# Performance work log

Measured on AMD Instinct MI355X. Metric: run time of the kernel, lower is better.

The kernel has to match this reference:

```python
import jax, jax.numpy as jnp
import numpy as np
import math


def setup_inputs() -> dict:
    key = jax.random.key(0)
    k1, k2, k3 = jax.random.split(key, 3)
    B, H, T, D = 4, 16, 4096, 128
    return {
        "q": jax.random.normal(k1, (B, H, T, D), dtype=jnp.float32),
        "k": jax.random.normal(k2, (B, H, T, D), dtype=jnp.float32),
        "v": jax.random.normal(k3, (B, H, T, D), dtype=jnp.float32),
        "BS": 32,
    }


def _compress(x, block_size):
    # blockwise mean-pool along T: [B,H,T,D] -> [B,H,C,D], C = ceil(T/BS)
    B, H, T, D = x.shape
    C = math.ceil(T / block_size)
    pad = C * block_size - T
    if pad:
        x = jnp.pad(x, ((0, 0), (0, 0), (0, pad), (0, 0)))
    return x.reshape(B, H, C, block_size, D).mean(axis=3)


def reference(q, k, v, BS):
    dk = k.shape[-1]
    k_cmp = _compress(k, BS)  # [B,H,C,D]
    v_cmp = _compress(v, BS)  # [B,H,C,D]
    # scaled dot-product attention over compressed KV
    score = jnp.einsum("bhtd,bhcd->bhtc", q, k_cmp) / math.sqrt(dk)
    score = jax.nn.softmax(score, axis=-1)  # [B,H,T,C]
    out = jnp.einsum("bhtc,bhcd->bhtd", score, v_cmp)  # [B,H,T,D]
    return (out, score)
```

## Files before the change

kernel.cpp:

```cpp
#include <hip/hip_runtime.h>
#include <hip/hip_bf16.h>

typedef __attribute__((ext_vector_type(8))) short short8;
typedef __attribute__((ext_vector_type(4))) float f32x4;

#define B_  4
#define H_  16
#define T_  4096
#define D_  128
#define BS_ 32
#define C_  128
#define BH_ (B_ * H_)

__device__ __forceinline__ int posperm(int x) {
  return (x & ~31) | (((x >> 2) & 3) << 3) | (((x >> 4) & 1) << 2) | (x & 3);
}

__device__ __forceinline__ unsigned short f2bf(float f) {
  __hip_bfloat16 h = __float2bfloat16(f);
  return __builtin_bit_cast(unsigned short, h);
}

__device__ __forceinline__ void gload_lds16(const uint4* g, uint4* l) {
  __builtin_amdgcn_global_load_lds(
      (const __attribute__((address_space(1))) unsigned int*)g,
      (__attribute__((address_space(3))) unsigned int*)l, 16, 0, 0);
}

__global__ __launch_bounds__(256) void compress_kernel(
    const float* __restrict__ k, const float* __restrict__ v,
    unsigned short* __restrict__ kc, unsigned short* __restrict__ vT) {
  int blk = blockIdx.x;
  int bh  = blk >> 4;
  int cg  = blk & 15;
  int cb  = cg * 8 + (threadIdx.x >> 5);
  int l   = threadIdx.x & 31;
  const float* kp = k + ((size_t)bh * T_ + (size_t)cb * BS_) * D_ + 4 * l;
  const float* vp = v + ((size_t)bh * T_ + (size_t)cb * BS_) * D_ + 4 * l;
  float4 ks = {0.f, 0.f, 0.f, 0.f}, vs = {0.f, 0.f, 0.f, 0.f};
#pragma unroll
  for (int j = 0; j < BS_; ++j) {
    float4 a = *(const float4*)(kp + (size_t)j * D_);
    float4 b = *(const float4*)(vp + (size_t)j * D_);
    ks.x += a.x; ks.y += a.y; ks.z += a.z; ks.w += a.w;
    vs.x += b.x; vs.y += b.y; vs.z += b.z; vs.w += b.w;
  }
  const float s  = 1.0f / BS_;
  const float sk = s * 0.08838834764831845f;
  size_t slab = (size_t)bh * (C_ * D_);
  unsigned short kq[4] = {f2bf(ks.x * sk), f2bf(ks.y * sk), f2bf(ks.z * sk), f2bf(ks.w * sk)};
  int p0 = posperm(4 * l) ^ ((cb & 7) << 3);
  *(uint2*)&kc[slab + (size_t)cb * D_ + p0] = *(const uint2*)kq;
  float vv[4] = {vs.x * s, vs.y * s, vs.z * s, vs.w * s};
#pragma unroll
  for (int i = 0; i < 4; ++i) {
    int d = 4 * l + i;
    vT[slab + (size_t)d * C_ + (posperm(cb) ^ ((d & 7) << 3))] = f2bf(vv[i]);
  }
}

__global__ __launch_bounds__(256, 4) void attn_kernel(
    const float* __restrict__ q, const unsigned short* __restrict__ kc,
    const unsigned short* __restrict__ vT, float* __restrict__ out,
    float* __restrict__ score) {
  __shared__ uint4 sbuf[2048];

  int blk    = blockIdx.x;
  int bh     = blk >> 6;
  int tchunk = blk & 63;
  int tid    = threadIdx.x;
  int wave   = tid >> 6;
  int lane   = tid & 63;
  int g      = lane >> 4;
  int lr     = lane & 15;
  int rx     = lr & 7;
  int t0     = tchunk * 64 + wave * 16;

  const uint4* kg = (const uint4*)(kc + (size_t)bh * (C_ * D_));
  const uint4* vg = (const uint4*)(vT + (size_t)bh * (C_ * D_));

  const float* qrow = q + ((size_t)bh * T_ + t0 + lr) * D_;
  float4 qa[4], qb[4];
#pragma unroll
  for (int ks = 0; ks < 4; ++ks) {
    int d0 = 4 * g + 32 * ks;
    qa[ks] = *(const float4*)(qrow + d0);
    qb[ks] = *(const float4*)(qrow + d0 + 16);
  }

#pragma unroll
  for (int it = 0; it < 8; ++it) gload_lds16(&kg[it * 256 + tid], &sbuf[it * 256 + tid]);

  short8 qf[4];
#pragma unroll
  for (int ks = 0; ks < 4; ++ks) {
    short8 f;
    f[0] = (short)f2bf(qa[ks].x); f[1] = (short)f2bf(qa[ks].y);
    f[2] = (short)f2bf(qa[ks].z); f[3] = (short)f2bf(qa[ks].w);
    f[4] = (short)f2bf(qb[ks].x); f[5] = (short)f2bf(qb[ks].y);
    f[6] = (short)f2bf(qb[ks].z); f[7] = (short)f2bf(qb[ks].w);
    qf[ks] = f;
  }
  __syncthreads();

  f32x4 accS[8];
#pragma unroll
  for (int cm = 0; cm < 8; ++cm) accS[cm] = f32x4{0.f, 0.f, 0.f, 0.f};
#pragma unroll
  for (int cm = 0; cm < 8; ++cm) {
    int rbase = (lr + 16 * cm) * 16;
#pragma unroll
    for (int ks = 0; ks < 4; ++ks) {
      uint4 kf = sbuf[rbase + ((4 * ks + g) ^ rx)];
      accS[cm] = __builtin_amdgcn_mfma_f32_16x16x32_bf16(
          __builtin_bit_cast(short8, kf), qf[ks], accS[cm], 0, 0, 0);
    }
  }

  float m = -3.0e38f;
#pragma unroll
  for (int cm = 0; cm < 8; ++cm)
#pragma unroll
    for (int r = 0; r < 4; ++r) m = fmaxf(m, accS[cm][r]);
  m = fmaxf(m, __shfl_xor(m, 16));
  m = fmaxf(m, __shfl_xor(m, 32));

  float sum = 0.f;
#pragma unroll
  for (int cm = 0; cm < 8; ++cm) {
#pragma unroll
    for (int r = 0; r < 4; ++r) {
      float p = __expf(accS[cm][r] - m);
      accS[cm][r] = p;
      sum += p;
    }
  }
  sum += __shfl_xor(sum, 16);
  sum += __shfl_xor(sum, 32);
  float inv = 1.0f / sum;
#pragma unroll
  for (int cm = 0; cm < 8; ++cm)
#pragma unroll
    for (int r = 0; r < 4; ++r) accS[cm][r] *= inv;

  __syncthreads();

  float* bw = (float*)sbuf + wave * 2048;
#pragma unroll
  for (int cm = 0; cm < 8; ++cm) {
    int c4 = (g + 4 * cm) ^ rx;
    *(f32x4*)&bw[lr * 128 + c4 * 4] = accS[cm];
  }
  float* dstS = score + ((size_t)bh * T_ + t0) * C_;
#pragma unroll
  for (int j = 0; j < 8; ++j) {
    int row = 2 * j + (lane >> 5);
    int c4  = lane & 31;
    f32x4 val = *(const f32x4*)&bw[row * 128 + (c4 ^ (row & 7)) * 4];
    __builtin_nontemporal_store(val, (f32x4*)&dstS[(size_t)row * C_ + c4 * 4]);
  }

  short8 pf[4];
#pragma unroll
  for (int ks = 0; ks < 4; ++ks) {
    short8 f;
#pragma unroll
    for (int r = 0; r < 4; ++r) {
      f[r]     = (short)f2bf(accS[2 * ks][r]);
      f[4 + r] = (short)f2bf(accS[2 * ks + 1][r]);
    }
    pf[ks] = f;
  }
  __syncthreads();

#pragma unroll
  for (int it = 0; it < 8; ++it) gload_lds16(&vg[it * 256 + tid], &sbuf[it * 256 + tid]);
  __syncthreads();

  f32x4 o[8];
#pragma unroll
  for (int nt = 0; nt < 8; ++nt) o[nt] = f32x4{0.f, 0.f, 0.f, 0.f};
#pragma unroll
  for (int nt = 0; nt < 8; ++nt) {
    int rbase = (lr + 16 * nt) * 16;
#pragma unroll
    for (int ks = 0; ks < 4; ++ks) {
      uint4 vf = sbuf[rbase + ((4 * ks + g) ^ rx)];
      o[nt] = __builtin_amdgcn_mfma_f32_16x16x32_bf16(
          __builtin_bit_cast(short8, vf), pf[ks], o[nt], 0, 0, 0);
    }
  }
  __syncthreads();

#pragma unroll
  for (int nt = 0; nt < 8; ++nt) {
    int c4 = (g + 4 * nt) ^ rx;
    *(f32x4*)&bw[lr * 128 + c4 * 4] = o[nt];
  }
  float* dstO = out + ((size_t)bh * T_ + t0) * D_;
#pragma unroll
  for (int j = 0; j < 8; ++j) {
    int row = 2 * j + (lane >> 5);
    int c4  = lane & 31;
    f32x4 val = *(const f32x4*)&bw[row * 128 + (c4 ^ (row & 7)) * 4];
    __builtin_nontemporal_store(val, (f32x4*)&dstO[(size_t)row * D_ + c4 * 4]);
  }
}

extern "C" void kernel_launch(void* const* d_in, const int* in_sizes, int n_in,
                              void* d_out, int out_size, void* d_ws, size_t ws_size,
                              hipStream_t stream) {
  const float* q = (const float*)d_in[0];
  const float* k = (const float*)d_in[1];
  const float* v = (const float*)d_in[2];
  float* out   = (float*)d_out;
  float* score = out + (size_t)BH_ * T_ * D_;

  unsigned short* kc = (unsigned short*)d_ws;
  unsigned short* vT = kc + (size_t)BH_ * C_ * D_;

  compress_kernel<<<BH_ * 16, 256, 0, stream>>>(k, v, kc, vT);
  attn_kernel<<<BH_ * 64, 256, 0, stream>>>(q, kc, vT, out, score);
}
```

Before: 128.0 us.

## Store score/out directly from MFMA registers and overlap V load with score stores

```diff
diff --git a/kernel.cpp b/kernel.cpp
--- a/kernel.cpp
+++ b/kernel.cpp
@@ -145,20 +145,16 @@
 
   __syncthreads();
 
-  float* bw = (float*)sbuf + wave * 2048;
+#pragma unroll
+  for (int it = 0; it < 8; ++it) gload_lds16(&vg[it * 256 + tid], &sbuf[it * 256 + tid]);
+  __builtin_amdgcn_sched_barrier(0);
+
+  float* dstS = score + ((size_t)bh * T_ + t0 + lr) * C_;
 #pragma unroll
   for (int cm = 0; cm < 8; ++cm) {
-    int c4 = (g + 4 * cm) ^ rx;
-    *(f32x4*)&bw[lr * 128 + c4 * 4] = accS[cm];
-  }
-  float* dstS = score + ((size_t)bh * T_ + t0) * C_;
-#pragma unroll
-  for (int j = 0; j < 8; ++j) {
-    int row = 2 * j + (lane >> 5);
-    int c4  = lane & 31;
-    f32x4 val = *(const f32x4*)&bw[row * 128 + (c4 ^ (row & 7)) * 4];
-    __builtin_nontemporal_store(val, (f32x4*)&dstS[(size_t)row * C_ + c4 * 4]);
-  }
+    __builtin_nontemporal_store(accS[cm], (f32x4*)&dstS[16 * cm + 4 * g]);
+  }
+  __builtin_amdgcn_sched_barrier(0);
 
   short8 pf[4];
 #pragma unroll
@@ -171,39 +167,23 @@
     }
     pf[ks] = f;
   }
-  __syncthreads();
-
-#pragma unroll
-  for (int it = 0; it < 8; ++it) gload_lds16(&vg[it * 256 + tid], &sbuf[it * 256 + tid]);
-  __syncthreads();
-
-  f32x4 o[8];
-#pragma unroll
-  for (int nt = 0; nt < 8; ++nt) o[nt] = f32x4{0.f, 0.f, 0.f, 0.f};
+
+  asm volatile("s_waitcnt vmcnt(8)" ::: "memory");
+  __builtin_amdgcn_s_barrier();
+  __builtin_amdgcn_sched_barrier(0);
+
+  float* dstO = out + ((size_t)bh * T_ + t0 + lr) * D_;
 #pragma unroll
   for (int nt = 0; nt < 8; ++nt) {
+    f32x4 o = f32x4{0.f, 0.f, 0.f, 0.f};
     int rbase = (lr + 16 * nt) * 16;
 #pragma unroll
     for (int ks = 0; ks < 4; ++ks) {
       uint4 vf = sbuf[rbase + ((4 * ks + g) ^ rx)];
-      o[nt] = __builtin_amdgcn_mfma_f32_16x16x32_bf16(
-          __builtin_bit_cast(short8, vf), pf[ks], o[nt], 0, 0, 0);
-    }
-  }
-  __syncthreads();
-
-#pragma unroll
-  for (int nt = 0; nt < 8; ++nt) {
-    int c4 = (g + 4 * nt) ^ rx;
-    *(f32x4*)&bw[lr * 128 + c4 * 4] = o[nt];
-  }
-  float* dstO = out + ((size_t)bh * T_ + t0) * D_;
-#pragma unroll
-  for (int j = 0; j < 8; ++j) {
-    int row = 2 * j + (lane >> 5);
-    int c4  = lane & 31;
-    f32x4 val = *(const f32x4*)&bw[row * 128 + (c4 ^ (row & 7)) * 4];
-    __builtin_nontemporal_store(val, (f32x4*)&dstO[(size_t)row * D_ + c4 * 4]);
+      o = __builtin_amdgcn_mfma_f32_16x16x32_bf16(
+          __builtin_bit_cast(short8, vf), pf[ks], o, 0, 0, 0);
+    }
+    __builtin_nontemporal_store(o, (f32x4*)&dstO[16 * nt + 4 * g]);
   }
 }
 
```

Measured after the change: 138.3 us. +8.1%, slower.
